# Optimization experiments

Hardware: AMD Instinct MI355X
Metric: run time of the kernel (lower is better)

Reference implementation:

```python
import jax, jax.numpy as jnp
import numpy as np

T, B, N, L = 4, 8, 25000, 64
D_IN = 1 + 2 * L  # node_dim + latent + time_dim


def setup_inputs() -> dict:
    key = jax.random.key(0)
    ks = jax.random.split(key, 20)
    f = lambda k, shp, s=0.1: jax.random.normal(k, shp, dtype=jnp.float32) * s
    z = lambda shp: jnp.zeros(shp, jnp.float32)
    return dict(
        raw=f(ks[0], (T, B, N, 1), 1.0),
        r_label=f(ks[1], (T, B, N, 1), 1.0),
        t=jax.random.uniform(ks[2], (T, B, N, 1), dtype=jnp.float32) * 100.0,
        src=jax.random.randint(ks[3], (T, B), 0, N, dtype=jnp.int32),
        tar=jax.random.randint(ks[4], (T, B), 0, N, dtype=jnp.int32),
        n_mask=jax.random.randint(ks[5], (T, B, N), 0, 2, dtype=jnp.int32),
        w_t=f(ks[6], (L,)), b_t=f(ks[7], (L,)),
        W_msg=f(ks[8], (1 + L, L)), b_msg=z((L,)),
        Wi=f(ks[9], (L, 3 * L)), Wh=f(ks[10], (L, 3 * L)),
        bi=z((3 * L,)), bh=z((3 * L,)),
        Wq=f(ks[11], (D_IN, L)), bq=z((L,)),
        Wk=f(ks[12], (D_IN, L)), bk=z((L,)),
        Wv=f(ks[13], (D_IN, L)), bv=z((L,)),
        W_out=f(ks[14], (L, 1)), b_out=z((1,)),
    )


def reference(raw, r_label, t, src, tar, n_mask, w_t, b_t, W_msg, b_msg,
              Wi, Wh, bi, bh, Wq, bq, Wk, bk, Wv, bv, W_out, b_out):
    Ldim = w_t.shape[0]
    Bdim, Ndim = raw.shape[1], raw.shape[2]
    bidx = jnp.arange(Bdim)
    scale = 1.0 / jnp.sqrt(jnp.float32(Ldim))
    enc0 = jnp.cos(b_t)  # time encoding of t=0 for the target query

    def time_enc(tt):  # [..., 1] -> [..., L]
        return jnp.cos(tt * w_t + b_t)

    def gru(x, h):  # torch.nn.GRUCell math
        gi = x @ Wi + bi
        gh = h @ Wh + bh
        ir, iz, inn = jnp.split(gi, 3, axis=-1)
        hr, hz, hn = jnp.split(gh, 3, axis=-1)
        rg = jax.nn.sigmoid(ir + hr)
        zg = jax.nn.sigmoid(iz + hz)
        ng = jnp.tanh(inn + rg * hn)
        return (1.0 - zg) * ng + zg * h

    def step(carry, inp):
        memory, r = carry            # [N,L], [B,N,1]
        t_b, tar_b, mask_b, rlab_b = inp  # [B,N,1], [B], [B,N], [N,1]
        enc_t = time_enc(t_b)        # [B,N,L]
        # 1. memory update (message from last batch element, GRU over all nodes)
        msg = jnp.concatenate([r[-1], enc_t[-1]], axis=-1) @ W_msg + b_msg  # [N,L]
        mem2 = gru(msg, memory)      # [N,L]
        # 2. embedding: target query over all node features
        tar_r = r[bidx, tar_b]       # [B,1]
        tar_hid = mem2[tar_b]        # [B,L]
        tar_h = jnp.concatenate(
            [tar_r, tar_hid, jnp.broadcast_to(enc0, (Bdim, Ldim))], axis=-1)  # [B,1+2L]
        h = jnp.concatenate(
            [r, jnp.broadcast_to(mem2[None], (Bdim, Ndim, Ldim)), enc_t], axis=-1)  # [B,N,1+2L]
        q = tar_h @ Wq + bq          # [B,L]
        k = h @ Wk + bk              # [B,N,L]
        v = h @ Wv + bv              # [B,N,L]
        scores = jnp.einsum('bl,bnl->bn', q, k) * scale
        scores = jnp.where(mask_b > 0, scores, jnp.float32(-1e9))
        attn = jax.nn.softmax(scores, axis=-1)
        z = jnp.einsum('bn,bnl->bl', attn, v)  # [B,L]
        logit = z @ W_out + b_out    # [B,1]
        # vectorized scatter replacing the python loop r_pred[tar_id]=pred_logit
        r_pred = r[-1].at[tar_b].set(logit)    # [N,1]
        r_last = 0.5 * (r_pred + rlab_b)       # teacher forcing blend
        r_next = jnp.broadcast_to(r_last[None], (Bdim, Ndim, 1))
        return (mem2, r_next), logit

    mem0 = jnp.zeros((Ndim, Ldim), jnp.float32)
    rlab_last = r_label[:, -1]  # [T,N,1]
    (_, _), logits = jax.lax.scan(step, (mem0, raw[0]), (t, tar, n_mask, rlab_last))
    return logits  # [T,B,1]
```

## Files before the change

kernel.cpp:

```cpp
#include <hip/hip_runtime.h>
#include <math.h>

#define TSTEPS 4
#define BB 8
#define NN 25000
#define LLD 64
#define DIN 129

#define OFF_W6    0
#define OFF_I4    24576
#define OFF_R4    24832
#define OFF_A     25088
#define OFF_WQ0   33473
#define OFF_CA    33602
#define OFF_C0Q   33667
#define OFF_WVO   33668
#define OFF_C0    33797
#define OFF_BFRAG 36864
#define OFF_MEMA  73728
#define OFF_MEMB  1673728
#define OFF_RLAST 3273728
#define OFF_PART  3298728
#define NBLK 98
#define PSTRIDE 132

typedef short s16x8 __attribute__((ext_vector_type(8)));
typedef float f32x4 __attribute__((ext_vector_type(4)));

__device__ __forceinline__ float sigm(float x) { return 1.f / (1.f + __expf(-x)); }
__device__ __forceinline__ float tanh_fast(float x) {
  float ax = fabsf(x);
  float e = __expf(-2.f * ax);
  float t = (1.f - e) / (1.f + e);
  return copysignf(t, x);
}
__device__ __forceinline__ float wred_max(float v) {
#pragma unroll
  for (int m = 32; m; m >>= 1) v = fmaxf(v, __shfl_xor(v, m));
  return v;
}
__device__ __forceinline__ float wred_sum(float v) {
#pragma unroll
  for (int m = 32; m; m >>= 1) v += __shfl_xor(v, m);
  return v;
}
__device__ __forceinline__ unsigned short bf16_rne(float v) {
  unsigned int u = __float_as_uint(v);
  unsigned int r = (u + 0x7FFFu + ((u >> 16) & 1u)) >> 16;
  return (unsigned short)r;
}
__device__ __forceinline__ float bf16_to_f(unsigned short b) {
  return __uint_as_float(((unsigned int)b) << 16);
}

__global__ __launch_bounds__(1024) void k_setup(
    const float* __restrict__ W_msg, const float* __restrict__ Wi,
    const float* __restrict__ bi, const float* __restrict__ b_msg,
    const float* __restrict__ bh, const float* __restrict__ Wh,
    const float* __restrict__ Wq, const float* __restrict__ bq,
    const float* __restrict__ Wk, const float* __restrict__ bk,
    const float* __restrict__ Wv, const float* __restrict__ bv,
    const float* __restrict__ W_out, const float* __restrict__ b_out,
    const float* __restrict__ b_t, float* __restrict__ ws) {
  if (blockIdx.x == 0) {
    __shared__ float u_lds[64];
    int tid = threadIdx.x;
    if (tid < 64) {
      float acc = bq[tid];
      for (int l = 0; l < 64; l++) acc += __cosf(b_t[l]) * Wq[(65 + l) * 64 + tid];
      u_lds[tid] = acc;
    }
    __syncthreads();
    if (tid < 129) {
      float acc = 0.f;
      for (int j = 0; j < 64; j++) acc += Wk[tid * 64 + j] * u_lds[j];
      ws[OFF_WQ0 + tid] = acc;
    } else if (tid == 129) {
      float acc = 0.f;
      for (int j = 0; j < 64; j++) acc += bk[j] * u_lds[j];
      ws[OFF_C0Q] = acc;
    }
    return;
  }
  int id = (blockIdx.x - 1) * 1024 + threadIdx.x;
  if (id < 24576) {
    int k = id / 384, rem = id % 384, l = rem / 6, g = rem % 6;
    float acc = 0.f;
    if (g < 3) {
      for (int m = 0; m < 64; m++) acc += W_msg[(k + 1) * 64 + m] * Wi[m * 192 + g * 64 + l];
    } else {
      acc = Wh[k * 192 + (g - 3) * 64 + l];
    }
    ws[OFF_W6 + id] = acc;
  } else if (id < 24832) {
    int id2 = id - 24576, l = id2 / 4, g = id2 % 4;
    float v;
    if (g == 3) v = bh[128 + l];
    else {
      int j = g * 64 + l;
      float bcf = bi[j];
      for (int m = 0; m < 64; m++) bcf += b_msg[m] * Wi[m * 192 + j];
      v = (g < 2) ? (bcf + bh[j]) : bcf;
    }
    ws[OFF_I4 + id2] = v;
  } else if (id < 25088) {
    int id2 = id - 24832, l = id2 / 4, g = id2 % 4;
    float v = 0.f;
    if (g < 3) {
      for (int m = 0; m < 64; m++) v += W_msg[m] * Wi[m * 192 + g * 64 + l];
    }
    ws[OFF_R4 + id2] = v;
  } else if (id < 33473) {
    int id3 = id - 25088, d = id3 / 65, i = id3 % 65;
    float acc = 0.f;
    for (int j = 0; j < 64; j++) acc += Wk[d * 64 + j] * Wq[i * 64 + j];
    ws[OFF_A + id3] = acc;
  } else if (id < 33538) {
    int i = id - 33473;
    float acc = 0.f;
    for (int j = 0; j < 64; j++) acc += bk[j] * Wq[i * 64 + j];
    ws[OFF_CA + i] = acc;
  } else if (id < 33667) {
    int d = id - 33538;
    float acc = 0.f;
    for (int j = 0; j < 64; j++) acc += Wv[d * 64 + j] * W_out[j];
    ws[OFF_WVO + d] = acc;
  } else if (id == 33667) {
    float acc = b_out[0];
    for (int j = 0; j < 64; j++) acc += bv[j] * W_out[j];
    ws[OFF_C0] = acc;
  }
}

__global__ __launch_bounds__(1024) void k_pack(
    const float* __restrict__ ws_r, float* __restrict__ ws) {
  int id = blockIdx.x * 1024 + threadIdx.x;
  int r = id & 7, lane = (id >> 3) & 63, kt = (id >> 9) & 3, ct = id >> 11;
  int col = 16 * ct + (lane & 15);
  int k = 32 * kt + ((lane >> 4) << 3) + r;
  int a = col >> 6, l = col & 63;
  float w = 0.f;
  if (k < 64) {
    if (a < 3) w = ws_r[OFF_W6 + (k * 64 + l) * 6 + a];
  } else {
    int k2 = k - 64;
    if (a == 0) w = ws_r[OFF_W6 + (k2 * 64 + l) * 6 + 3];
    else if (a == 1) w = ws_r[OFF_W6 + (k2 * 64 + l) * 6 + 4];
    else if (a == 3) w = ws_r[OFF_W6 + (k2 * 64 + l) * 6 + 5];
  }
  unsigned short hb = bf16_rne(w);
  unsigned short lb = bf16_rne(w - bf16_to_f(hb));
  unsigned short* BFu = (unsigned short*)(ws + OFF_BFRAG);
  int idx = ((ct * 4 + kt) * 64 + lane) * 8 + r;
  BFu[idx] = hb;
  BFu[32768 + idx] = lb;
}

__global__ __launch_bounds__(256, 2) void k_gru(
    const float* __restrict__ t_in, const float* __restrict__ raw,
    const float* __restrict__ r_in, const float* __restrict__ w_t,
    const float* __restrict__ b_t, const float* __restrict__ i4p,
    const float* __restrict__ r4p, const unsigned short* __restrict__ BF,
    const float* __restrict__ memPrev, float* __restrict__ memNext, int tt) {
  __shared__ unsigned short XhiS[64 * 136];
  __shared__ unsigned short XloS[64 * 136];
  __shared__ float tb_lds[64], rn_lds[64];
  int tid = threadIdx.x;
  int lane = tid & 63;
  int wv = tid >> 6;
  int nbase = blockIdx.x * 64;

  if (tid < 64) {
    int nc = min(nbase + tid, NN - 1);
    tb_lds[tid] = t_in[(tt * BB + BB - 1) * NN + nc];
    rn_lds[tid] = (tt == 0) ? raw[(BB - 1) * NN + nc] : r_in[nc];
  }
  __syncthreads();

  {
    int nl = lane;
    int nc = min(nbase + nl, NN - 1);
    float tb = tb_lds[nl];
    int swz = (nl & 7) << 3;
    const float4* mp4 = (const float4*)(memPrev + (size_t)nc * 64);
#pragma unroll
    for (int c = 0; c < 4; c++) {
      int kc = wv * 32 + c * 8;
      float vv[8];
      if (kc < 64) {
#pragma unroll
        for (int j = 0; j < 8; j++) vv[j] = __cosf(tb * w_t[kc + j] + b_t[kc + j]);
      } else if (tt == 0) {
#pragma unroll
        for (int j = 0; j < 8; j++) vv[j] = 0.f;
      } else {
        int d0 = kc - 64;
        float4 f0 = mp4[d0 >> 2];
        float4 f1 = mp4[(d0 >> 2) + 1];
        vv[0] = f0.x; vv[1] = f0.y; vv[2] = f0.z; vv[3] = f0.w;
        vv[4] = f1.x; vv[5] = f1.y; vv[6] = f1.z; vv[7] = f1.w;
      }
      s16x8 h8, l8;
#pragma unroll
      for (int j = 0; j < 8; j++) {
        unsigned short hb = bf16_rne(vv[j]);
        h8[j] = (short)hb;
        l8[j] = (short)bf16_rne(vv[j] - bf16_to_f(hb));
      }
      int off = nl * 136 + (kc ^ swz);
      *(s16x8*)(XhiS + off) = h8;
      *(s16x8*)(XloS + off) = l8;
    }
  }
  __syncthreads();

  const s16x8* BF8 = (const s16x8*)BF;
  f32x4 acc[4][4];
#pragma unroll
  for (int g = 0; g < 4; g++)
#pragma unroll
    for (int m = 0; m < 4; m++) acc[g][m] = (f32x4){0.f, 0.f, 0.f, 0.f};

  int swzA = (lane & 7) << 3;
#pragma unroll
  for (int kt = 0; kt < 4; kt++) {
    s16x8 bh[4], bl[4];
#pragma unroll
    for (int g = 0; g < 4; g++) {
      int ct = wv + 4 * g;
      bh[g] = BF8[(ct * 4 + kt) * 64 + lane];
      bl[g] = BF8[4096 + (ct * 4 + kt) * 64 + lane];
    }
#pragma unroll
    for (int m = 0; m < 4; m++) {
      int row = 16 * m + (lane & 15);
      int off = row * 136 + ((32 * kt + 8 * (lane >> 4)) ^ swzA);
      s16x8 ah = *(const s16x8*)(XhiS + off);
      s16x8 al = *(const s16x8*)(XloS + off);
#pragma unroll
      for (int g = 0; g < 4; g++) {
        acc[g][m] = __builtin_amdgcn_mfma_f32_16x16x32_bf16(ah, bh[g], acc[g][m], 0, 0, 0);
        acc[g][m] = __builtin_amdgcn_mfma_f32_16x16x32_bf16(ah, bl[g], acc[g][m], 0, 0, 0);
        acc[g][m] = __builtin_amdgcn_mfma_f32_16x16x32_bf16(al, bh[g], acc[g][m], 0, 0, 0);
      }
    }
  }

  int myl = 16 * wv + (lane & 15);
  float4 iv = ((const float4*)i4p)[myl];
  float4 rv = ((const float4*)r4p)[myl];
  int kmem = 64 + myl;
  int slot = kmem & ~7;
  int wel = kmem & 7;
#pragma unroll
  for (int m = 0; m < 4; m++) {
#pragma unroll
    for (int i = 0; i < 4; i++) {
      int nloc = 16 * m + (lane >> 4) * 4 + i;
      float rn = rn_lds[nloc];
      float gRv = acc[0][m][i] + iv.x + rn * rv.x;
      float gZv = acc[1][m][i] + iv.y + rn * rv.y;
      float aNv = acc[2][m][i] + iv.z + rn * rv.z;
      float hNv = acc[3][m][i] + iv.w;
      float rg = sigm(gRv);
      float zg = sigm(gZv);
      float ng = tanh_fast(aNv + rg * hNv);
      int offm = nloc * 136 + (slot ^ ((nloc & 7) << 3)) + wel;
      float mp = bf16_to_f(XhiS[offm]) + bf16_to_f(XloS[offm]);
      int n = nbase + nloc;
      if (n < NN) memNext[(size_t)n * 64 + myl] = (1.f - zg) * ng + zg * mp;
    }
  }
}

__global__ __launch_bounds__(256) void k_attn(
    const float* __restrict__ t_in, const float* __restrict__ raw,
    const float* __restrict__ r_last, const int* __restrict__ n_mask,
    const float* __restrict__ w_t, const float* __restrict__ b_t,
    const int* __restrict__ tar, const float* __restrict__ A,
    const float* __restrict__ wq0, const float* __restrict__ cA,
    const float* __restrict__ c0q, const float* __restrict__ mem2,
    float* __restrict__ part, int tt) {
  __shared__ float m2t[64];
  __shared__ float wq_lds[132];
  __shared__ float e_sh[256], t_sh[256];
  __shared__ float red4[4], redS[4], redR[4];
  __shared__ float pm[2][64], pe[2][64];

  int tid = threadIdx.x;
  int lane = tid & 63;
  int wvid = tid >> 6;
  int b = blockIdx.y;
  int n0 = blockIdx.x * 256;
  int n = n0 + tid;
  int nc = min(n, NN - 1);
  bool valid = (n < NN);
  int tarn = tar[tt * BB + b];

  if (tid < 64) m2t[tid] = mem2[(size_t)tarn * 64 + tid];
  __syncthreads();
  float tr = (tt == 0) ? raw[b * NN + tarn] : r_last[tarn];
  if (tid < 129) {
    const float* Ar = A + tid * 65;
    float acc = wq0[tid] + tr * Ar[0];
#pragma unroll 8
    for (int k = 0; k < 64; k++) acc += m2t[k] * Ar[1 + k];
    wq_lds[tid] = acc;
  } else if (tid == 129) {
    float acc = c0q[0] + tr * cA[0];
    for (int k = 0; k < 64; k++) acc += m2t[k] * cA[1 + k];
    wq_lds[129] = acc;
  }

  float tb = t_in[(tt * BB + b) * NN + nc];
  int mk = n_mask[(tt * BB + b) * NN + nc];
  float rn = (tt == 0) ? raw[b * NN + nc] : r_last[nc];
  __syncthreads();

  float sc = rn * wq_lds[0];
  const float4* m4 = (const float4*)(mem2 + (size_t)nc * 64);
#pragma unroll
  for (int q = 0; q < 16; q++) {
    float4 v = m4[q];
    sc += v.x * wq_lds[1 + 4 * q] + v.y * wq_lds[2 + 4 * q] +
          v.z * wq_lds[3 + 4 * q] + v.w * wq_lds[4 + 4 * q];
  }
#pragma unroll 8
  for (int l = 0; l < 64; l++) sc += __cosf(tb * w_t[l] + b_t[l]) * wq_lds[65 + l];
  float score = (sc + wq_lds[129]) * 0.125f;
  bool act = valid && (mk > 0);

  float mw = wred_max(act ? score : -1e30f);
  if (lane == 0) red4[wvid] = mw;
  __syncthreads();
  float mb = fmaxf(fmaxf(red4[0], red4[1]), fmaxf(red4[2], red4[3]));

  float e = act ? __expf(score - mb) : 0.f;
  float sw = wred_sum(e);
  float sr = wred_sum(e * rn);
  if (lane == 0) { redS[wvid] = sw; redR[wvid] = sr; }
  e_sh[tid] = e;
  t_sh[tid] = tb;
  __syncthreads();
  float Sb = redS[0] + redS[1] + redS[2] + redS[3];
  float Rb = redR[0] + redR[1] + redR[2] + redR[3];

  if (wvid < 2) {
    int i0 = wvid * 128;
    float acc = 0.f;
#pragma unroll 4
    for (int i = i0; i < i0 + 128; i++) {
      int ii = min(n0 + i, NN - 1);
      acc += e_sh[i] * mem2[(size_t)ii * 64 + lane];
    }
    pm[wvid][lane] = acc;
  } else {
    float wl = w_t[lane], bl = b_t[lane];
    int i0 = (wvid - 2) * 128;
    float acc = 0.f;
#pragma unroll 4
    for (int i = i0; i < i0 + 128; i++) acc += e_sh[i] * __cosf(t_sh[i] * wl + bl);
    pe[wvid - 2][lane] = acc;
  }
  __syncthreads();

  int pbase = (b * NBLK + blockIdx.x) * PSTRIDE;
  if (tid < 64) part[pbase + 1 + tid] = pm[0][tid] + pm[1][tid];
  else if (tid < 128) part[pbase + 65 + (tid - 64)] = pe[0][tid - 64] + pe[1][tid - 64];
  else if (tid == 128) part[pbase + 0] = Rb;
  else if (tid == 129) part[pbase + 129] = mb;
  else if (tid == 130) part[pbase + 130] = Sb;
}

__global__ __launch_bounds__(256) void k_merge(
    const float* __restrict__ part, const float* __restrict__ wvo,
    const float* __restrict__ c0p, const int* __restrict__ tar,
    const float* __restrict__ raw, const float* __restrict__ r_label,
    float* __restrict__ r_last, float* __restrict__ out, int tt) {
  int tid = threadIdx.x;
  if (blockIdx.x < NBLK) {
    int n = blockIdx.x * 256 + tid;
    if (n >= NN) return;
    bool istar = false;
#pragma unroll
    for (int b = 0; b < BB; b++) istar |= (tar[tt * BB + b] == n);
    if (istar) return;
    float base = (tt == 0) ? raw[(BB - 1) * NN + n] : r_last[n];
    r_last[n] = 0.5f * (base + r_label[(tt * BB + BB - 1) * NN + n]);
    return;
  }

  int b = blockIdx.x - NBLK;
  const float* pb = part + b * NBLK * PSTRIDE;
  __shared__ float red[256], fac[NBLK];

  red[tid] = (tid < NBLK) ? pb[tid * PSTRIDE + 129] : -1e30f;
  __syncthreads();
  for (int s = 128; s > 0; s >>= 1) {
    if (tid < s) red[tid] = fmaxf(red[tid], red[tid + s]);
    __syncthreads();
  }
  float mb = red[0];
  __syncthreads();
  if (tid < NBLK) fac[tid] = __expf(pb[tid * PSTRIDE + 129] - mb);
  __syncthreads();
  red[tid] = (tid < NBLK) ? pb[tid * PSTRIDE + 130] * fac[tid] : 0.f;
  __syncthreads();
  for (int s = 128; s > 0; s >>= 1) {
    if (tid < s) red[tid] += red[tid + s];
    __syncthreads();
  }
  float Sb = red[0];
  __syncthreads();

  float acc = 0.f;
  if (tid < DIN) {
    float a0 = 0.f, a1 = 0.f, a2 = 0.f, a3 = 0.f;
    int j = 0;
    for (; j + 3 < NBLK; j += 4) {
      a0 += fac[j] * pb[j * PSTRIDE + tid];
      a1 += fac[j + 1] * pb[(j + 1) * PSTRIDE + tid];
      a2 += fac[j + 2] * pb[(j + 2) * PSTRIDE + tid];
      a3 += fac[j + 3] * pb[(j + 3) * PSTRIDE + tid];
    }
    for (; j < NBLK; j++) a0 += fac[j] * pb[j * PSTRIDE + tid];
    acc = ((a0 + a1) + (a2 + a3)) * wvo[tid];
  }
  red[tid] = (tid < DIN) ? acc : 0.f;
  __syncthreads();
  for (int s = 128; s > 0; s >>= 1) {
    if (tid < s) red[tid] += red[tid + s];
    __syncthreads();
  }
  if (tid == 0) {
    float lg = red[0] / Sb + c0p[0];
    out[tt * BB + b] = lg;
    int mytar = tar[tt * BB + b];
    bool last = true;
    for (int bb = b + 1; bb < BB; bb++)
      if (tar[tt * BB + bb] == mytar) last = false;
    if (last)
      r_last[mytar] = 0.5f * (lg + r_label[(tt * BB + BB - 1) * NN + mytar]);
  }
}

extern "C" void kernel_launch(void* const* d_in, const int* in_sizes, int n_in,
                              void* d_out, int out_size, void* d_ws, size_t ws_size,
                              hipStream_t stream) {
  const float* raw     = (const float*)d_in[0];
  const float* r_label = (const float*)d_in[1];
  const float* t_in    = (const float*)d_in[2];
  const int*   tar     = (const int*)d_in[4];
  const int*   n_mask  = (const int*)d_in[5];
  const float* w_t     = (const float*)d_in[6];
  const float* b_t     = (const float*)d_in[7];
  const float* W_msg   = (const float*)d_in[8];
  const float* b_msg   = (const float*)d_in[9];
  const float* Wi      = (const float*)d_in[10];
  const float* Wh      = (const float*)d_in[11];
  const float* bi      = (const float*)d_in[12];
  const float* bh      = (const float*)d_in[13];
  const float* Wq      = (const float*)d_in[14];
  const float* bq      = (const float*)d_in[15];
  const float* Wk      = (const float*)d_in[16];
  const float* bk      = (const float*)d_in[17];
  const float* Wv      = (const float*)d_in[18];
  const float* bv      = (const float*)d_in[19];
  const float* W_out   = (const float*)d_in[20];
  const float* b_out   = (const float*)d_in[21];

  float* ws  = (float*)d_ws;
  float* out = (float*)d_out;

  k_setup<<<34, 1024, 0, stream>>>(W_msg, Wi, bi, b_msg, bh, Wh, Wq, bq, Wk, bk,
                                   Wv, bv, W_out, b_out, b_t, ws);
  k_pack<<<32, 1024, 0, stream>>>(ws, ws);

  for (int tt = 0; tt < TSTEPS; tt++) {
    float* mp = ws + ((tt & 1) ? OFF_MEMB : OFF_MEMA);
    float* mn = ws + ((tt & 1) ? OFF_MEMA : OFF_MEMB);
    k_gru<<<dim3((NN + 63) / 64), dim3(256), 0, stream>>>(
        t_in, raw, ws + OFF_RLAST, w_t, b_t,
        ws + OFF_I4, ws + OFF_R4, (const unsigned short*)(ws + OFF_BFRAG),
        mp, mn, tt);
    k_attn<<<dim3(NBLK, BB), dim3(256), 0, stream>>>(
        t_in, raw, ws + OFF_RLAST, n_mask, w_t, b_t, tar,
        ws + OFF_A, ws + OFF_WQ0, ws + OFF_CA, ws + OFF_C0Q,
        mn, ws + OFF_PART, tt);
    k_merge<<<dim3(NBLK + BB), dim3(256), 0, stream>>>(
        ws + OFF_PART, ws + OFF_WVO, ws + OFF_C0, tar,
        raw, r_label, ws + OFF_RLAST, out, tt);
  }
}
```

Before: 194.9 us.

## Restructure attention into single-wave blocks with swizzled LDS memory tile

Changes k_attn from 256-thread blocks over 256 nodes to 64-thread single-wave blocks over 64 nodes, four times as many blocks. Each block stages its 64x64 memory rows into a swizzled LDS tile. The score dot product and the weighted value sum then both read from LDS instead of loading mem2 from global twice, and block-level syncs and cross-wave reductions go away. The cost is a fourfold larger partials array for k_merge to reduce, and the per-block recomputation of the 130-entry query projection now runs 4x more often across the grid, with each thread doing three dot products instead of roughly one.

```diff
diff --git a/kernel.cpp b/kernel.cpp
--- a/kernel.cpp
+++ b/kernel.cpp
@@ -21,7 +21,8 @@
 #define OFF_MEMB  1673728
 #define OFF_RLAST 3273728
 #define OFF_PART  3298728
-#define NBLK 98
+#define NBLK 392
+#define NBULK 98
 #define PSTRIDE 132
 
 typedef short s16x8 __attribute__((ext_vector_type(8)));
@@ -273,7 +274,7 @@
   }
 }
 
-__global__ __launch_bounds__(256) void k_attn(
+__global__ __launch_bounds__(64) void k_attn(
     const float* __restrict__ t_in, const float* __restrict__ raw,
     const float* __restrict__ r_last, const int* __restrict__ n_mask,
     const float* __restrict__ w_t, const float* __restrict__ b_t,
@@ -281,95 +282,84 @@
     const float* __restrict__ wq0, const float* __restrict__ cA,
     const float* __restrict__ c0q, const float* __restrict__ mem2,
     float* __restrict__ part, int tt) {
+  __shared__ float m2s[64][64];
   __shared__ float m2t[64];
   __shared__ float wq_lds[132];
-  __shared__ float e_sh[256], t_sh[256];
-  __shared__ float red4[4], redS[4], redR[4];
-  __shared__ float pm[2][64], pe[2][64];
-
-  int tid = threadIdx.x;
-  int lane = tid & 63;
-  int wvid = tid >> 6;
+  __shared__ float e_sh[64], t_sh[64];
+
+  int lane = threadIdx.x;
   int b = blockIdx.y;
-  int n0 = blockIdx.x * 256;
-  int n = n0 + tid;
+  int n0 = blockIdx.x * 64;
+  int n = n0 + lane;
   int nc = min(n, NN - 1);
   bool valid = (n < NN);
   int tarn = tar[tt * BB + b];
 
-  if (tid < 64) m2t[tid] = mem2[(size_t)tarn * 64 + tid];
-  __syncthreads();
+#pragma unroll
+  for (int k = 0; k < 16; k++) {
+    int fi = k * 64 + lane;
+    int row = fi >> 4, slot = fi & 15;
+    int grow = min(n0 + row, NN - 1);
+    float4 v = ((const float4*)(mem2 + (size_t)grow * 64))[slot];
+    *(float4*)&m2s[row][(slot ^ (row & 15)) * 4] = v;
+  }
+  m2t[lane] = mem2[(size_t)tarn * 64 + lane];
+
   float tr = (tt == 0) ? raw[b * NN + tarn] : r_last[tarn];
-  if (tid < 129) {
-    const float* Ar = A + tid * 65;
-    float acc = wq0[tid] + tr * Ar[0];
+  for (int d = lane; d < 130; d += 64) {
+    float acc;
+    if (d < 129) {
+      const float* Ar = A + d * 65;
+      acc = wq0[d] + tr * Ar[0];
 #pragma unroll 8
-    for (int k = 0; k < 64; k++) acc += m2t[k] * Ar[1 + k];
-    wq_lds[tid] = acc;
-  } else if (tid == 129) {
-    float acc = c0q[0] + tr * cA[0];
-    for (int k = 0; k < 64; k++) acc += m2t[k] * cA[1 + k];
-    wq_lds[129] = acc;
+      for (int k = 0; k < 64; k++) acc += m2t[k] * Ar[1 + k];
+    } else {
+      acc = c0q[0] + tr * cA[0];
+      for (int k = 0; k < 64; k++) acc += m2t[k] * cA[1 + k];
+    }
+    wq_lds[d] = acc;
   }
 
   float tb = t_in[(tt * BB + b) * NN + nc];
   int mk = n_mask[(tt * BB + b) * NN + nc];
   float rn = (tt == 0) ? raw[b * NN + nc] : r_last[nc];
-  __syncthreads();
 
   float sc = rn * wq_lds[0];
-  const float4* m4 = (const float4*)(mem2 + (size_t)nc * 64);
-#pragma unroll
-  for (int q = 0; q < 16; q++) {
-    float4 v = m4[q];
-    sc += v.x * wq_lds[1 + 4 * q] + v.y * wq_lds[2 + 4 * q] +
-          v.z * wq_lds[3 + 4 * q] + v.w * wq_lds[4 + 4 * q];
+#pragma unroll
+  for (int s = 0; s < 16; s++) {
+    float4 v = *(const float4*)&m2s[lane][(s ^ (lane & 15)) * 4];
+    sc += v.x * wq_lds[1 + 4 * s] + v.y * wq_lds[2 + 4 * s] +
+          v.z * wq_lds[3 + 4 * s] + v.w * wq_lds[4 + 4 * s];
   }
 #pragma unroll 8
   for (int l = 0; l < 64; l++) sc += __cosf(tb * w_t[l] + b_t[l]) * wq_lds[65 + l];
   float score = (sc + wq_lds[129]) * 0.125f;
   bool act = valid && (mk > 0);
 
-  float mw = wred_max(act ? score : -1e30f);
-  if (lane == 0) red4[wvid] = mw;
-  __syncthreads();
-  float mb = fmaxf(fmaxf(red4[0], red4[1]), fmaxf(red4[2], red4[3]));
-
+  float mb = wred_max(act ? score : -1e30f);
   float e = act ? __expf(score - mb) : 0.f;
-  float sw = wred_sum(e);
-  float sr = wred_sum(e * rn);
-  if (lane == 0) { redS[wvid] = sw; redR[wvid] = sr; }
-  e_sh[tid] = e;
-  t_sh[tid] = tb;
-  __syncthreads();
-  float Sb = redS[0] + redS[1] + redS[2] + redS[3];
-  float Rb = redR[0] + redR[1] + redR[2] + redR[3];
-
-  if (wvid < 2) {
-    int i0 = wvid * 128;
-    float acc = 0.f;
+  float Sb = wred_sum(e);
+  float Rb = wred_sum(e * rn);
+  e_sh[lane] = e;
+  t_sh[lane] = tb;
+
+  float pmAcc = 0.f;
 #pragma unroll 4
-    for (int i = i0; i < i0 + 128; i++) {
-      int ii = min(n0 + i, NN - 1);
-      acc += e_sh[i] * mem2[(size_t)ii * 64 + lane];
-    }
-    pm[wvid][lane] = acc;
-  } else {
-    float wl = w_t[lane], bl = b_t[lane];
-    int i0 = (wvid - 2) * 128;
-    float acc = 0.f;
+  for (int i = 0; i < 64; i++) {
+    float v = m2s[i][(((lane >> 2) ^ (i & 15)) << 2) + (lane & 3)];
+    pmAcc += e_sh[i] * v;
+  }
+  float wl = w_t[lane], bl = b_t[lane];
+  float peAcc = 0.f;
 #pragma unroll 4
-    for (int i = i0; i < i0 + 128; i++) acc += e_sh[i] * __cosf(t_sh[i] * wl + bl);
-    pe[wvid - 2][lane] = acc;
-  }
-  __syncthreads();
+  for (int i = 0; i < 64; i++) peAcc += e_sh[i] * __cosf(t_sh[i] * wl + bl);
 
   int pbase = (b * NBLK + blockIdx.x) * PSTRIDE;
-  if (tid < 64) part[pbase + 1 + tid] = pm[0][tid] + pm[1][tid];
-  else if (tid < 128) part[pbase + 65 + (tid - 64)] = pe[0][tid - 64] + pe[1][tid - 64];
-  else if (tid == 128) part[pbase + 0] = Rb;
-  else if (tid == 129) part[pbase + 129] = mb;
-  else if (tid == 130) part[pbase + 130] = Sb;
+  part[pbase + 1 + lane] = pmAcc;
+  part[pbase + 65 + lane] = peAcc;
+  if (lane == 0) part[pbase + 0] = Rb;
+  else if (lane == 1) part[pbase + 129] = mb;
+  else if (lane == 2) part[pbase + 130] = Sb;
 }
 
 __global__ __launch_bounds__(256) void k_merge(
@@ -378,7 +368,7 @@
     const float* __restrict__ raw, const float* __restrict__ r_label,
     float* __restrict__ r_last, float* __restrict__ out, int tt) {
   int tid = threadIdx.x;
-  if (blockIdx.x < NBLK) {
+  if (blockIdx.x < NBULK) {
     int n = blockIdx.x * 256 + tid;
     if (n >= NN) return;
     bool istar = false;
@@ -390,11 +380,15 @@
     return;
   }
 
-  int b = blockIdx.x - NBLK;
+  int b = blockIdx.x - NBULK;
   const float* pb = part + b * NBLK * PSTRIDE;
   __shared__ float red[256], fac[NBLK];
 
-  red[tid] = (tid < NBLK) ? pb[tid * PSTRIDE + 129] : -1e30f;
+  {
+    float m1 = pb[tid * PSTRIDE + 129];
+    float m2v = (tid + 256 < NBLK) ? pb[(tid + 256) * PSTRIDE + 129] : -1e30f;
+    red[tid] = fmaxf(m1, m2v);
+  }
   __syncthreads();
   for (int s = 128; s > 0; s >>= 1) {
     if (tid < s) red[tid] = fmaxf(red[tid], red[tid + s]);
@@ -402,9 +396,13 @@
   }
   float mb = red[0];
   __syncthreads();
-  if (tid < NBLK) fac[tid] = __expf(pb[tid * PSTRIDE + 129] - mb);
-  __syncthreads();
-  red[tid] = (tid < NBLK) ? pb[tid * PSTRIDE + 130] * fac[tid] : 0.f;
+  for (int j = tid; j < NBLK; j += 256) fac[j] = __expf(pb[j * PSTRIDE + 129] - mb);
+  __syncthreads();
+  {
+    float s1 = pb[tid * PSTRIDE + 130] * fac[tid];
+    if (tid + 256 < NBLK) s1 += pb[(tid + 256) * PSTRIDE + 130] * fac[tid + 256];
+    red[tid] = s1;
+  }
   __syncthreads();
   for (int s = 128; s > 0; s >>= 1) {
     if (tid < s) red[tid] += red[tid + s];
@@ -483,11 +481,11 @@
         t_in, raw, ws + OFF_RLAST, w_t, b_t,
         ws + OFF_I4, ws + OFF_R4, (const unsigned short*)(ws + OFF_BFRAG),
         mp, mn, tt);
-    k_attn<<<dim3(NBLK, BB), dim3(256), 0, stream>>>(
+    k_attn<<<dim3(NBLK, BB), dim3(64), 0, stream>>>(
         t_in, raw, ws + OFF_RLAST, n_mask, w_t, b_t, tar,
         ws + OFF_A, ws + OFF_WQ0, ws + OFF_CA, ws + OFF_C0Q,
         mn, ws + OFF_PART, tt);
-    k_merge<<<dim3(NBLK + BB), dim3(256), 0, stream>>>(
+    k_merge<<<dim3(NBULK + BB), dim3(256), 0, stream>>>(
         ws + OFF_PART, ws + OFF_WVO, ws + OFF_C0, tar,
         raw, r_label, ws + OFF_RLAST, out, tt);
   }
```

Measured after the change: 264.4 us. +35.7%, slower.

## Compute per-target query weights in GRU kernel and split attention reduction across all waves

Applied to the files above, without the earlier changes.

The folded query vector (wq) for each batch target is now computed once by the GRU block owning that target node and written to workspace. Previously every one of the 98x8 attention blocks recomputed it, a serial 129x64 matvec. The attention value reduction is also rebalanced so all four waves handle both the memory-weighted sum and the time-encoding sum, with eight independent accumulators for more memory-level parallelism. In exchange, the GRU kernel gains extra syncthreads loops, and it relies on the memNext writes of the same block being visible after a barrier.

```diff
diff --git a/kernel.cpp b/kernel.cpp
--- a/kernel.cpp
+++ b/kernel.cpp
@@ -16,6 +16,7 @@
 #define OFF_C0Q   33667
 #define OFF_WVO   33668
 #define OFF_C0    33797
+#define OFF_WQC   33856
 #define OFF_BFRAG 36864
 #define OFF_MEMA  73728
 #define OFF_MEMB  1673728
@@ -161,10 +162,14 @@
     const float* __restrict__ r_in, const float* __restrict__ w_t,
     const float* __restrict__ b_t, const float* __restrict__ i4p,
     const float* __restrict__ r4p, const unsigned short* __restrict__ BF,
-    const float* __restrict__ memPrev, float* __restrict__ memNext, int tt) {
+    const float* __restrict__ memPrev, float* __restrict__ memNext,
+    const int* __restrict__ tar, const float* __restrict__ A,
+    const float* __restrict__ wq0, const float* __restrict__ cA,
+    const float* __restrict__ c0q, float* __restrict__ wqc, int tt) {
   __shared__ unsigned short XhiS[64 * 136];
   __shared__ unsigned short XloS[64 * 136];
   __shared__ float tb_lds[64], rn_lds[64];
+  __shared__ float q_lds[64];
   int tid = threadIdx.x;
   int lane = tid & 63;
   int wv = tid >> 6;
@@ -271,21 +276,39 @@
       if (n < NN) memNext[(size_t)n * 64 + myl] = (1.f - zg) * ng + zg * mp;
     }
   }
+
+  for (int b = 0; b < BB; b++) {
+    int tn = tar[tt * BB + b];
+    if ((tn >> 6) != (int)blockIdx.x) continue;
+    __syncthreads();
+    if (tid < 64) q_lds[tid] = memNext[(size_t)tn * 64 + tid];
+    __syncthreads();
+    float tr = (tt == 0) ? raw[b * NN + tn] : r_in[tn];
+    if (tid < 129) {
+      const float* Ar = A + tid * 65;
+      float acc2 = wq0[tid] + tr * Ar[0];
+#pragma unroll 8
+      for (int k = 0; k < 64; k++) acc2 += q_lds[k] * Ar[1 + k];
+      wqc[b * 132 + tid] = acc2;
+    } else if (tid == 129) {
+      float acc2 = c0q[0] + tr * cA[0];
+      for (int k = 0; k < 64; k++) acc2 += q_lds[k] * cA[1 + k];
+      wqc[b * 132 + 129] = acc2;
+    }
+    __syncthreads();
+  }
 }
 
 __global__ __launch_bounds__(256) void k_attn(
     const float* __restrict__ t_in, const float* __restrict__ raw,
     const float* __restrict__ r_last, const int* __restrict__ n_mask,
     const float* __restrict__ w_t, const float* __restrict__ b_t,
-    const int* __restrict__ tar, const float* __restrict__ A,
-    const float* __restrict__ wq0, const float* __restrict__ cA,
-    const float* __restrict__ c0q, const float* __restrict__ mem2,
+    const float* __restrict__ wqc, const float* __restrict__ mem2,
     float* __restrict__ part, int tt) {
-  __shared__ float m2t[64];
   __shared__ float wq_lds[132];
   __shared__ float e_sh[256], t_sh[256];
   __shared__ float red4[4], redS[4], redR[4];
-  __shared__ float pm[2][64], pe[2][64];
+  __shared__ float pmw[4][64], pew[4][64];
 
   int tid = threadIdx.x;
   int lane = tid & 63;
@@ -295,22 +318,8 @@
   int n = n0 + tid;
   int nc = min(n, NN - 1);
   bool valid = (n < NN);
-  int tarn = tar[tt * BB + b];
-
-  if (tid < 64) m2t[tid] = mem2[(size_t)tarn * 64 + tid];
-  __syncthreads();
-  float tr = (tt == 0) ? raw[b * NN + tarn] : r_last[tarn];
-  if (tid < 129) {
-    const float* Ar = A + tid * 65;
-    float acc = wq0[tid] + tr * Ar[0];
-#pragma unroll 8
-    for (int k = 0; k < 64; k++) acc += m2t[k] * Ar[1 + k];
-    wq_lds[tid] = acc;
-  } else if (tid == 129) {
-    float acc = c0q[0] + tr * cA[0];
-    for (int k = 0; k < 64; k++) acc += m2t[k] * cA[1 + k];
-    wq_lds[129] = acc;
-  }
+
+  if (tid < 130) wq_lds[tid] = wqc[b * 132 + tid];
 
   float tb = t_in[(tt * BB + b) * NN + nc];
   int mk = n_mask[(tt * BB + b) * NN + nc];
@@ -345,28 +354,37 @@
   float Sb = redS[0] + redS[1] + redS[2] + redS[3];
   float Rb = redR[0] + redR[1] + redR[2] + redR[3];
 
-  if (wvid < 2) {
-    int i0 = wvid * 128;
-    float acc = 0.f;
+  {
+    int ib = wvid * 64;
+    float a0 = 0.f, a1 = 0.f, a2 = 0.f, a3 = 0.f;
+    float a4 = 0.f, a5 = 0.f, a6 = 0.f, a7 = 0.f;
+#pragma unroll 2
+    for (int i = 0; i < 64; i += 8) {
+      int i0 = ib + i;
+      a0 += e_sh[i0 + 0] * mem2[(size_t)min(n0 + i0 + 0, NN - 1) * 64 + lane];
+      a1 += e_sh[i0 + 1] * mem2[(size_t)min(n0 + i0 + 1, NN - 1) * 64 + lane];
+      a2 += e_sh[i0 + 2] * mem2[(size_t)min(n0 + i0 + 2, NN - 1) * 64 + lane];
+      a3 += e_sh[i0 + 3] * mem2[(size_t)min(n0 + i0 + 3, NN - 1) * 64 + lane];
+      a4 += e_sh[i0 + 4] * mem2[(size_t)min(n0 + i0 + 4, NN - 1) * 64 + lane];
+      a5 += e_sh[i0 + 5] * mem2[(size_t)min(n0 + i0 + 5, NN - 1) * 64 + lane];
+      a6 += e_sh[i0 + 6] * mem2[(size_t)min(n0 + i0 + 6, NN - 1) * 64 + lane];
+      a7 += e_sh[i0 + 7] * mem2[(size_t)min(n0 + i0 + 7, NN - 1) * 64 + lane];
+    }
+    pmw[wvid][lane] = ((a0 + a1) + (a2 + a3)) + ((a4 + a5) + (a6 + a7));
+    float wl = w_t[lane], bl = b_t[lane];
+    float peA = 0.f;
 #pragma unroll 4
-    for (int i = i0; i < i0 + 128; i++) {
-      int ii = min(n0 + i, NN - 1);
-      acc += e_sh[i] * mem2[(size_t)ii * 64 + lane];
-    }
-    pm[wvid][lane] = acc;
-  } else {
-    float wl = w_t[lane], bl = b_t[lane];
-    int i0 = (wvid - 2) * 128;
-    float acc = 0.f;
-#pragma unroll 4
-    for (int i = i0; i < i0 + 128; i++) acc += e_sh[i] * __cosf(t_sh[i] * wl + bl);
-    pe[wvid - 2][lane] = acc;
+    for (int i = 0; i < 64; i++) peA += e_sh[ib + i] * __cosf(t_sh[ib + i] * wl + bl);
+    pew[wvid][lane] = peA;
   }
   __syncthreads();
 
   int pbase = (b * NBLK + blockIdx.x) * PSTRIDE;
-  if (tid < 64) part[pbase + 1 + tid] = pm[0][tid] + pm[1][tid];
-  else if (tid < 128) part[pbase + 65 + (tid - 64)] = pe[0][tid - 64] + pe[1][tid - 64];
+  if (tid < 64) part[pbase + 1 + tid] = (pmw[0][tid] + pmw[1][tid]) + (pmw[2][tid] + pmw[3][tid]);
+  else if (tid < 128) {
+    int d = tid - 64;
+    part[pbase + 65 + d] = (pew[0][d] + pew[1][d]) + (pew[2][d] + pew[3][d]);
+  }
   else if (tid == 128) part[pbase + 0] = Rb;
   else if (tid == 129) part[pbase + 129] = mb;
   else if (tid == 130) part[pbase + 130] = Sb;
@@ -482,11 +500,11 @@
     k_gru<<<dim3((NN + 63) / 64), dim3(256), 0, stream>>>(
         t_in, raw, ws + OFF_RLAST, w_t, b_t,
         ws + OFF_I4, ws + OFF_R4, (const unsigned short*)(ws + OFF_BFRAG),
-        mp, mn, tt);
+        mp, mn, tar, ws + OFF_A, ws + OFF_WQ0, ws + OFF_CA, ws + OFF_C0Q,
+        ws + OFF_WQC, tt);
     k_attn<<<dim3(NBLK, BB), dim3(256), 0, stream>>>(
-        t_in, raw, ws + OFF_RLAST, n_mask, w_t, b_t, tar,
-        ws + OFF_A, ws + OFF_WQ0, ws + OFF_CA, ws + OFF_C0Q,
-        mn, ws + OFF_PART, tt);
+        t_in, raw, ws + OFF_RLAST, n_mask, w_t, b_t,
+        ws + OFF_WQC, mn, ws + OFF_PART, tt);
     k_merge<<<dim3(NBLK + BB), dim3(256), 0, stream>>>(
         ws + OFF_PART, ws + OFF_WVO, ws + OFF_C0, tar,
         raw, r_label, ws + OFF_RLAST, out, tt);
```

Result: faster. 182.1 us (-6.6%).
